# Performance work log

Measured on AMD Instinct MI355X. Metric: run time of the kernel, lower is better.

## Reference

```python
import jax, jax.numpy as jnp
import numpy as np

IN_F = 128
OUT_F = 128
ALPHA = 0.2  # LeakyReLU negative slope


def _xavier_uniform(key, shape, gain):
    fan_in, fan_out = shape[0], shape[1]
    bound = gain * np.sqrt(6.0 / (fan_in + fan_out))
    return jax.random.uniform(key, shape, jnp.float32, -bound, bound)


def setup_inputs() -> dict:
    key = jax.random.key(0)
    kx, kw, ka = jax.random.split(key, 3)
    x = jax.random.normal(kx, (8, 2048, IN_F), jnp.float32)
    W = _xavier_uniform(kw, (IN_F, OUT_F), 1.414)
    a = _xavier_uniform(ka, (2 * OUT_F, 1), 1.414)
    return {"x": x, "W": W, "a": a}


def reference(x, W, a):
    B, T, _ = x.shape
    h = jnp.matmul(x, W)  # [B, T, F]
    # e_ij = leakyrelu([h_i ; h_j] @ a) = leakyrelu(h_i @ a1 + h_j @ a2)
    a1 = a[:OUT_F, 0]   # [F]
    a2 = a[OUT_F:, 0]   # [F]
    f1 = h @ a1         # [B, T]
    f2 = h @ a2         # [B, T]
    e = f1[:, :, None] + f2[:, None, :]          # [B, T, T]
    e = jnp.where(e >= 0, e, ALPHA * e)          # LeakyReLU
    attention = jax.nn.softmax(e, axis=-1)       # [B, T, T]
    # dropout is identity at inference
    return jnp.matmul(attention, h)              # [B, T, F]
```

## Files before the change

kernel.cpp:

```cpp
#include <hip/hip_runtime.h>
#include <hip/hip_bf16.h>

typedef __attribute__((ext_vector_type(8))) short short8;
typedef __attribute__((ext_vector_type(8))) unsigned short ushort8;
typedef __attribute__((ext_vector_type(16))) float f32x16;

#define LOG2E 1.4426950408889634f
#define MFMA32(a, b, c) __builtin_amdgcn_mfma_f32_32x32x16_bf16((a), (b), (c), 0, 0, 0)
#define ZERO16 {0.f,0.f,0.f,0.f,0.f,0.f,0.f,0.f,0.f,0.f,0.f,0.f,0.f,0.f,0.f,0.f}

__device__ __forceinline__ unsigned short bfbits(float f) {
    __hip_bfloat16 h = __float2bfloat16(f);
    return __builtin_bit_cast(unsigned short, h);
}
__device__ __forceinline__ float bf2f(unsigned short u) {
    unsigned v = ((unsigned)u) << 16;
    return __builtin_bit_cast(float, v);
}

__global__ __launch_bounds__(256) void gat_wt(const float* __restrict__ W,
                                              unsigned short* __restrict__ WT2h,
                                              unsigned short* __restrict__ WT2l,
                                              unsigned int* __restrict__ f2mk) {
    if (blockIdx.x == 0 && threadIdx.x < 8) f2mk[threadIdx.x] = 0u;
    const int k16 = blockIdx.x;
    const int d = threadIdx.x >> 1;
    const int klo8 = (threadIdx.x & 1) * 8;
    ushort8 vh, vl;
#pragma unroll
    for (int q = 0; q < 8; ++q) {
        float f = W[(k16 * 16 + klo8 + q) * 128 + d];
        unsigned short hb = bfbits(f);
        vh[q] = hb;
        vl[q] = bfbits(f - bf2f(hb));
    }
    size_t base = (size_t)k16 * 2048 + d * 16 + klo8;
    *(ushort8*)(WT2h + base) = vh;
    *(ushort8*)(WT2l + base) = vl;
}

__global__ __launch_bounds__(256) void gat_h(const float* __restrict__ x,
                                             const unsigned short* __restrict__ WT2h,
                                             const unsigned short* __restrict__ WT2l,
                                             const float* __restrict__ a,
                                             unsigned short* __restrict__ HT2h,
                                             float* __restrict__ f1l,
                                             float* __restrict__ f2l,
                                             unsigned int* __restrict__ f2mk) {
    __shared__ unsigned short xs_h[32][132];
    __shared__ unsigned short xs_l[32][132];
    __shared__ float hs[32][130];
    __shared__ float red[2][32][8];
    const int tid = threadIdx.x;
    const int lane = tid & 63;
    const int wv = tid >> 6;
    const int l31 = lane & 31;
    const int hi = lane >> 5;
    const int t0 = blockIdx.x * 32;
    const int c0 = wv * 32;

#pragma unroll
    for (int r8 = 0; r8 < 4; ++r8) {
        int row = r8 * 8 + (tid >> 5);
        int c4 = (tid & 31) * 4;
        float4 v = *(const float4*)(x + (size_t)(t0 + row) * 128 + c4);
        float f[4] = {v.x, v.y, v.z, v.w};
#pragma unroll
        for (int q = 0; q < 4; ++q) {
            unsigned short hb = bfbits(f[q]);
            xs_h[row][c4 + q] = hb;
            xs_l[row][c4 + q] = bfbits(f[q] - bf2f(hb));
        }
    }
    __syncthreads();

    f32x16 p0 = ZERO16, p1 = ZERO16, p2 = ZERO16;
    const unsigned short* bph = WT2h + (c0 + l31) * 16 + 8 * hi;
    const unsigned short* bpl = WT2l + (c0 + l31) * 16 + 8 * hi;
#pragma unroll
    for (int kk8 = 0; kk8 < 8; ++kk8) {
        short8 ah = *(const short8*)&xs_h[l31][kk8 * 16 + 8 * hi];
        short8 al = *(const short8*)&xs_l[l31][kk8 * 16 + 8 * hi];
        short8 bh = __builtin_bit_cast(short8, *(const ushort8*)(bph + kk8 * 2048));
        short8 bl = __builtin_bit_cast(short8, *(const ushort8*)(bpl + kk8 * 2048));
        p0 = MFMA32(ah, bh, p0);
        p1 = MFMA32(al, bh, p1);
        p2 = MFMA32(ah, bl, p2);
    }
#pragma unroll
    for (int r = 0; r < 16; ++r) {
        int crow = (r & 3) + 8 * (r >> 2) + 4 * hi;
        hs[crow][c0 + l31] = p0[r] + p1[r] + p2[r];
    }
    __syncthreads();
    {
        const int d = tid & 127, half = tid >> 7;
        ushort8 h0, h1;
#pragma unroll
        for (int j = 0; j < 8; ++j) h0[j] = bfbits(hs[half * 16 + j][d]);
#pragma unroll
        for (int j = 0; j < 8; ++j) h1[j] = bfbits(hs[half * 16 + 8 + j][d]);
        const int b = t0 >> 11;
        const int tloc = t0 & 2047;
        size_t base = (size_t)b * 262144 + (size_t)(tloc / 16 + half) * 2048 + d * 16;
        *(ushort8*)(HT2h + base) = h0;
        *(ushort8*)(HT2h + base + 8) = h1;
    }
    {
        const int r = tid & 31, seg = tid >> 5;
        float s1 = 0.f, s2 = 0.f;
#pragma unroll
        for (int i = 0; i < 16; ++i) {
            float hv = hs[r][seg * 16 + i];
            s1 += hv * a[seg * 16 + i];
            s2 += hv * a[128 + seg * 16 + i];
        }
        red[0][r][seg] = s1;
        red[1][r][seg] = s2;
    }
    __syncthreads();
    if (tid < 32) {
        float s1 = 0.f, s2 = 0.f;
#pragma unroll
        for (int g = 0; g < 8; ++g) { s1 += red[0][tid][g]; s2 += red[1][tid][g]; }
        f1l[t0 + tid] = s1 * LOG2E;
        float f2v = s2 * LOG2E;
        f2l[t0 + tid] = f2v;
        float m = f2v;
#pragma unroll
        for (int o = 1; o < 32; o <<= 1) m = fmaxf(m, __shfl_xor(m, o, 32));
        if (tid == 0) {
            unsigned int bits = __builtin_bit_cast(unsigned int, m);
            unsigned int key = (bits & 0x80000000u) ? ~bits : (bits | 0x80000000u);
            atomicMax(f2mk + (t0 >> 11), key);
        }
    }
}

__global__ __launch_bounds__(512, 2) void gat_attn(const unsigned short* __restrict__ HT2h,
                                                   const float* __restrict__ f1l,
                                                   const float* __restrict__ f2l,
                                                   const unsigned int* __restrict__ f2mk,
                                                   float* __restrict__ out) {
    __shared__ float lred[4][64][132];
    __shared__ float sps[8][64];
    __shared__ float sinv[64];
    const int bid = blockIdx.x;
    const int b = bid & 7;
    const int tile = bid >> 3;
    const int tid = threadIdx.x;
    const int lane = tid & 63;
    const int wv = tid >> 6;
    const int l31 = lane & 31;
    const int hi = lane >> 5;
    const int koff = hi * 8;

    const unsigned int kk = f2mk[b];
    const unsigned int mbits = (kk & 0x80000000u) ? (kk & 0x7fffffffu) : ~kk;
    const float fm = __builtin_bit_cast(float, mbits);

    const int rowg = b * 2048 + tile * 64 + l31;
    const float f1m0 = f1l[rowg];
    const float f1m1 = f1l[rowg + 32];
    const float tm0 = f1m0 + fm, tm1 = f1m1 + fm;
    const float ml0 = fmaxf(tm0, 0.2f * tm0);
    const float ml1 = fmaxf(tm1, 0.2f * tm1);
    const float A0 = f1m0 - ml0, B0 = 0.2f * f1m0 - ml0;
    const float A1 = f1m1 - ml1, B1 = 0.2f * f1m1 - ml1;

    const int jbase = wv * 256;
    const float* f2b = f2l + b * 2048 + jbase;
    const unsigned short* ph = HT2h + (size_t)b * 262144
                             + (size_t)(jbase >> 4) * 2048 + l31 * 16 + koff;

    f32x16 acc[2][4] = {{ZERO16, ZERO16, ZERO16, ZERO16},
                        {ZERO16, ZERO16, ZERO16, ZERO16}};
    float sp0 = 0.f, sp1 = 0.f;

    uint4 vh0 = *(const uint4*)(ph);
    uint4 vh1 = *(const uint4*)(ph + 512);
    uint4 vh2 = *(const uint4*)(ph + 1024);
    uint4 vh3 = *(const uint4*)(ph + 1536);

    for (int it = 0; it < 16; ++it) {
        const unsigned short* pn = ph + (size_t)((it + 1) & 15) * 2048;
        uint4 nh0 = *(const uint4*)(pn);
        uint4 nh1 = *(const uint4*)(pn + 512);
        uint4 nh2 = *(const uint4*)(pn + 1024);
        uint4 nh3 = *(const uint4*)(pn + 1536);
        float4 fva = *(const float4*)(f2b + it * 16 + koff);
        float4 fvb = *(const float4*)(f2b + it * 16 + koff + 4);

        float fv[8] = {fva.x, fva.y, fva.z, fva.w, fvb.x, fvb.y, fvb.z, fvb.w};
        short8 af0, af1;
#pragma unroll
        for (int q = 0; q < 8; ++q) {
            float g = 0.2f * fv[q];
            float p0 = __builtin_amdgcn_exp2f(fmaxf(A0 + fv[q], B0 + g));
            float p1 = __builtin_amdgcn_exp2f(fmaxf(A1 + fv[q], B1 + g));
            sp0 += p0; sp1 += p1;
            af0[q] = (short)bfbits(p0);
            af1[q] = (short)bfbits(p1);
        }
        acc[0][0] = MFMA32(af0, __builtin_bit_cast(short8, vh0), acc[0][0]);
        acc[0][1] = MFMA32(af0, __builtin_bit_cast(short8, vh1), acc[0][1]);
        acc[0][2] = MFMA32(af0, __builtin_bit_cast(short8, vh2), acc[0][2]);
        acc[0][3] = MFMA32(af0, __builtin_bit_cast(short8, vh3), acc[0][3]);
        acc[1][0] = MFMA32(af1, __builtin_bit_cast(short8, vh0), acc[1][0]);
        acc[1][1] = MFMA32(af1, __builtin_bit_cast(short8, vh1), acc[1][1]);
        acc[1][2] = MFMA32(af1, __builtin_bit_cast(short8, vh2), acc[1][2]);
        acc[1][3] = MFMA32(af1, __builtin_bit_cast(short8, vh3), acc[1][3]);

        vh0 = nh0; vh1 = nh1; vh2 = nh2; vh3 = nh3;
    }

    sp0 += __shfl_xor(sp0, 32, 64);
    sp1 += __shfl_xor(sp1, 32, 64);
    if (lane < 32) { sps[wv][l31] = sp0; sps[wv][32 + l31] = sp1; }

    if (wv >= 4) {
#pragma unroll
        for (int r = 0; r < 16; ++r) {
            int crow = (r & 3) + 8 * (r >> 2) + 4 * hi;
#pragma unroll
            for (int s = 0; s < 2; ++s)
#pragma unroll
                for (int c = 0; c < 4; ++c)
                    lred[wv - 4][s * 32 + crow][c * 32 + l31] = acc[s][c][r];
        }
    }
    __syncthreads();
    if (wv < 4) {
#pragma unroll
        for (int r = 0; r < 16; ++r) {
            int crow = (r & 3) + 8 * (r >> 2) + 4 * hi;
#pragma unroll
            for (int s = 0; s < 2; ++s)
#pragma unroll
                for (int c = 0; c < 4; ++c)
                    acc[s][c][r] += lred[wv][s * 32 + crow][c * 32 + l31];
        }
    } else if (wv == 4) {
        float tot = 0.f;
#pragma unroll
        for (int w = 0; w < 8; ++w) tot += sps[w][lane];
        sinv[lane] = 1.0f / tot;
    }
    __syncthreads();
    if (wv == 2 || wv == 3) {
#pragma unroll
        for (int r = 0; r < 16; ++r) {
            int crow = (r & 3) + 8 * (r >> 2) + 4 * hi;
#pragma unroll
            for (int s = 0; s < 2; ++s)
#pragma unroll
                for (int c = 0; c < 4; ++c)
                    lred[wv - 2][s * 32 + crow][c * 32 + l31] = acc[s][c][r];
        }
    }
    __syncthreads();
    if (wv < 2) {
#pragma unroll
        for (int r = 0; r < 16; ++r) {
            int crow = (r & 3) + 8 * (r >> 2) + 4 * hi;
#pragma unroll
            for (int s = 0; s < 2; ++s)
#pragma unroll
                for (int c = 0; c < 4; ++c)
                    acc[s][c][r] += lred[wv][s * 32 + crow][c * 32 + l31];
        }
    }
    __syncthreads();
    if (wv == 1) {
#pragma unroll
        for (int r = 0; r < 16; ++r) {
            int crow = (r & 3) + 8 * (r >> 2) + 4 * hi;
#pragma unroll
            for (int s = 0; s < 2; ++s)
#pragma unroll
                for (int c = 0; c < 4; ++c)
                    lred[0][s * 32 + crow][c * 32 + l31] = acc[s][c][r];
        }
    }
    __syncthreads();
    if (wv == 0) {
        const size_t obase = ((size_t)b * 2048 + (size_t)tile * 64) * 128;
#pragma unroll
        for (int r = 0; r < 16; ++r) {
            int crow = (r & 3) + 8 * (r >> 2) + 4 * hi;
#pragma unroll
            for (int s = 0; s < 2; ++s) {
                int row = s * 32 + crow;
                float iv = sinv[row];
#pragma unroll
                for (int c = 0; c < 4; ++c) {
                    float v = acc[s][c][r] + lred[0][row][c * 32 + l31];
                    out[obase + (size_t)row * 128 + c * 32 + l31] = v * iv;
                }
            }
        }
    }
}

extern "C" void kernel_launch(void* const* d_in, const int* in_sizes, int n_in,
                              void* d_out, int out_size, void* d_ws, size_t ws_size,
                              hipStream_t stream) {
    const float* x = (const float*)d_in[0];
    const float* W = (const float*)d_in[1];
    const float* a = (const float*)d_in[2];
    float* out = (float*)d_out;

    unsigned short* WT2h = (unsigned short*)d_ws;
    unsigned short* WT2l = WT2h + 128 * 128;
    unsigned short* HT2h = WT2l + 128 * 128;
    float* f1l = (float*)(HT2h + (size_t)8 * 128 * 2048);
    float* f2l = f1l + 16384;
    unsigned int* f2mk = (unsigned int*)(f2l + 16384);

    gat_wt<<<8, 256, 0, stream>>>(W, WT2h, WT2l, f2mk);
    gat_h<<<512, 256, 0, stream>>>(x, WT2h, WT2l, a, HT2h, f1l, f2l, f2mk);
    gat_attn<<<256, 512, 0, stream>>>(HT2h, f1l, f2l, f2mk, out);
}
```

Measured before the change: 40.16 us.

## Stage f2 in LDS and double-buffer H loads across two unrolled iterations

The f2 row vector is copied once per block into shared memory so the inner loop reads it from LDS instead of global memory. The main loop is unrolled by two with separate X/Y register buffers, prefetching H two steps ahead and interleaving exp generation with MFMA issue. The lred padding is also dropped from 132 to 128, which may bring LDS bank conflicts back in the reduction. The aim is to hide global load latency and overlap VALU exp work with matrix ops, at the cost of more registers and extra LDS.

```diff
diff --git a/kernel.cpp b/kernel.cpp
--- a/kernel.cpp
+++ b/kernel.cpp
@@ -137,12 +137,29 @@
     }
 }
 
+__device__ __forceinline__ void gen_af(float4 fa, float4 fb,
+                                       float A0, float B0, float A1, float B1,
+                                       float& sp0, float& sp1,
+                                       short8& af0, short8& af1) {
+    float fv[8] = {fa.x, fa.y, fa.z, fa.w, fb.x, fb.y, fb.z, fb.w};
+#pragma unroll
+    for (int q = 0; q < 8; ++q) {
+        float g = 0.2f * fv[q];
+        float p0 = __builtin_amdgcn_exp2f(fmaxf(A0 + fv[q], B0 + g));
+        float p1 = __builtin_amdgcn_exp2f(fmaxf(A1 + fv[q], B1 + g));
+        sp0 += p0; sp1 += p1;
+        af0[q] = (short)bfbits(p0);
+        af1[q] = (short)bfbits(p1);
+    }
+}
+
 __global__ __launch_bounds__(512, 2) void gat_attn(const unsigned short* __restrict__ HT2h,
                                                    const float* __restrict__ f1l,
                                                    const float* __restrict__ f2l,
                                                    const unsigned int* __restrict__ f2mk,
                                                    float* __restrict__ out) {
-    __shared__ float lred[4][64][132];
+    __shared__ float lred[4][64][128];
+    __shared__ float f2s[2048];
     __shared__ float sps[8][64];
     __shared__ float sinv[64];
     const int bid = blockIdx.x;
@@ -155,6 +172,8 @@
     const int hi = lane >> 5;
     const int koff = hi * 8;
 
+    *(float4*)(f2s + tid * 4) = *(const float4*)(f2l + b * 2048 + tid * 4);
+
     const unsigned int kk = f2mk[b];
     const unsigned int mbits = (kk & 0x80000000u) ? (kk & 0x7fffffffu) : ~kk;
     const float fm = __builtin_bit_cast(float, mbits);
@@ -168,50 +187,71 @@
     const float A0 = f1m0 - ml0, B0 = 0.2f * f1m0 - ml0;
     const float A1 = f1m1 - ml1, B1 = 0.2f * f1m1 - ml1;
 
-    const int jbase = wv * 256;
-    const float* f2b = f2l + b * 2048 + jbase;
-    const unsigned short* ph = HT2h + (size_t)b * 262144
-                             + (size_t)(jbase >> 4) * 2048 + l31 * 16 + koff;
+    const int jloc = wv * 256;
+    const unsigned short* phg = HT2h + (size_t)b * 262144
+                              + (size_t)(jloc >> 4) * 2048 + l31 * 16 + koff;
 
     f32x16 acc[2][4] = {{ZERO16, ZERO16, ZERO16, ZERO16},
                         {ZERO16, ZERO16, ZERO16, ZERO16}};
     float sp0 = 0.f, sp1 = 0.f;
 
-    uint4 vh0 = *(const uint4*)(ph);
-    uint4 vh1 = *(const uint4*)(ph + 512);
-    uint4 vh2 = *(const uint4*)(ph + 1024);
-    uint4 vh3 = *(const uint4*)(ph + 1536);
-
-    for (int it = 0; it < 16; ++it) {
-        const unsigned short* pn = ph + (size_t)((it + 1) & 15) * 2048;
-        uint4 nh0 = *(const uint4*)(pn);
-        uint4 nh1 = *(const uint4*)(pn + 512);
-        uint4 nh2 = *(const uint4*)(pn + 1024);
-        uint4 nh3 = *(const uint4*)(pn + 1536);
-        float4 fva = *(const float4*)(f2b + it * 16 + koff);
-        float4 fvb = *(const float4*)(f2b + it * 16 + koff + 4);
-
-        float fv[8] = {fva.x, fva.y, fva.z, fva.w, fvb.x, fvb.y, fvb.z, fvb.w};
+    uint4 X0 = *(const uint4*)(phg);
+    uint4 X1 = *(const uint4*)(phg + 512);
+    uint4 X2 = *(const uint4*)(phg + 1024);
+    uint4 X3 = *(const uint4*)(phg + 1536);
+    uint4 Y0 = *(const uint4*)(phg + 2048);
+    uint4 Y1 = *(const uint4*)(phg + 2048 + 512);
+    uint4 Y2 = *(const uint4*)(phg + 2048 + 1024);
+    uint4 Y3 = *(const uint4*)(phg + 2048 + 1536);
+
+    __syncthreads();
+
+    float4 fA0 = *(const float4*)(f2s + jloc + koff);
+    float4 fA1 = *(const float4*)(f2s + jloc + koff + 4);
+
+    for (int it2 = 0; it2 < 8; ++it2) {
+        const int itE = it2 * 2, itO = it2 * 2 + 1;
         short8 af0, af1;
-#pragma unroll
-        for (int q = 0; q < 8; ++q) {
-            float g = 0.2f * fv[q];
-            float p0 = __builtin_amdgcn_exp2f(fmaxf(A0 + fv[q], B0 + g));
-            float p1 = __builtin_amdgcn_exp2f(fmaxf(A1 + fv[q], B1 + g));
-            sp0 += p0; sp1 += p1;
-            af0[q] = (short)bfbits(p0);
-            af1[q] = (short)bfbits(p1);
-        }
-        acc[0][0] = MFMA32(af0, __builtin_bit_cast(short8, vh0), acc[0][0]);
-        acc[0][1] = MFMA32(af0, __builtin_bit_cast(short8, vh1), acc[0][1]);
-        acc[0][2] = MFMA32(af0, __builtin_bit_cast(short8, vh2), acc[0][2]);
-        acc[0][3] = MFMA32(af0, __builtin_bit_cast(short8, vh3), acc[0][3]);
-        acc[1][0] = MFMA32(af1, __builtin_bit_cast(short8, vh0), acc[1][0]);
-        acc[1][1] = MFMA32(af1, __builtin_bit_cast(short8, vh1), acc[1][1]);
-        acc[1][2] = MFMA32(af1, __builtin_bit_cast(short8, vh2), acc[1][2]);
-        acc[1][3] = MFMA32(af1, __builtin_bit_cast(short8, vh3), acc[1][3]);
-
-        vh0 = nh0; vh1 = nh1; vh2 = nh2; vh3 = nh3;
+        gen_af(fA0, fA1, A0, B0, A1, B1, sp0, sp1, af0, af1);
+        float4 fB0 = *(const float4*)(f2s + jloc + itO * 16 + koff);
+        float4 fB1 = *(const float4*)(f2s + jloc + itO * 16 + koff + 4);
+        acc[0][0] = MFMA32(af0, __builtin_bit_cast(short8, X0), acc[0][0]);
+        acc[0][1] = MFMA32(af0, __builtin_bit_cast(short8, X1), acc[0][1]);
+        acc[0][2] = MFMA32(af0, __builtin_bit_cast(short8, X2), acc[0][2]);
+        acc[0][3] = MFMA32(af0, __builtin_bit_cast(short8, X3), acc[0][3]);
+        acc[1][0] = MFMA32(af1, __builtin_bit_cast(short8, X0), acc[1][0]);
+        acc[1][1] = MFMA32(af1, __builtin_bit_cast(short8, X1), acc[1][1]);
+        acc[1][2] = MFMA32(af1, __builtin_bit_cast(short8, X2), acc[1][2]);
+        acc[1][3] = MFMA32(af1, __builtin_bit_cast(short8, X3), acc[1][3]);
+        {
+            const unsigned short* pn = phg + (size_t)((itE + 2) & 15) * 2048;
+            X0 = *(const uint4*)(pn);
+            X1 = *(const uint4*)(pn + 512);
+            X2 = *(const uint4*)(pn + 1024);
+            X3 = *(const uint4*)(pn + 1536);
+        }
+        short8 bf0, bf1;
+        gen_af(fB0, fB1, A0, B0, A1, B1, sp0, sp1, bf0, bf1);
+        {
+            const int itN = (itO + 1) & 15;
+            fA0 = *(const float4*)(f2s + jloc + itN * 16 + koff);
+            fA1 = *(const float4*)(f2s + jloc + itN * 16 + koff + 4);
+        }
+        acc[0][0] = MFMA32(bf0, __builtin_bit_cast(short8, Y0), acc[0][0]);
+        acc[0][1] = MFMA32(bf0, __builtin_bit_cast(short8, Y1), acc[0][1]);
+        acc[0][2] = MFMA32(bf0, __builtin_bit_cast(short8, Y2), acc[0][2]);
+        acc[0][3] = MFMA32(bf0, __builtin_bit_cast(short8, Y3), acc[0][3]);
+        acc[1][0] = MFMA32(bf1, __builtin_bit_cast(short8, Y0), acc[1][0]);
+        acc[1][1] = MFMA32(bf1, __builtin_bit_cast(short8, Y1), acc[1][1]);
+        acc[1][2] = MFMA32(bf1, __builtin_bit_cast(short8, Y2), acc[1][2]);
+        acc[1][3] = MFMA32(bf1, __builtin_bit_cast(short8, Y3), acc[1][3]);
+        {
+            const unsigned short* pn = phg + (size_t)((itO + 2) & 15) * 2048;
+            Y0 = *(const uint4*)(pn);
+            Y1 = *(const uint4*)(pn + 512);
+            Y2 = *(const uint4*)(pn + 1024);
+            Y3 = *(const uint4*)(pn + 1536);
+        }
     }
 
     sp0 += __shfl_xor(sp0, 32, 64);
```

After: 38.89 us. -3.2%, faster.

## Stream H tiles through LDS with async global_load_lds ring buffer

Applied to the files above, without the earlier changes.

Replaces the per-wave register double-buffered global loads of the H tiles with a 4-deep ring of direct global-to-LDS async loads (global_load_lds), gated by vmcnt waits. It also stages the f2 logits for the batch into shared memory once per block, and reuses the new 128KB shared buffer for the cross-wave reduction. The aim is to hide global-memory latency deeper and cut register pressure. The costs are much larger LDS use (about 140KB per block), which may block the two-blocks-per-CU target, plus an extra barrier. There is also a risk that the slot being refilled is overwritten while its LDS reads may still be in flight.

```diff
diff --git a/kernel.cpp b/kernel.cpp
--- a/kernel.cpp
+++ b/kernel.cpp
@@ -16,6 +16,12 @@
 __device__ __forceinline__ float bf2f(unsigned short u) {
     unsigned v = ((unsigned)u) << 16;
     return __builtin_bit_cast(float, v);
+}
+
+typedef unsigned int __attribute__((address_space(1))) as1_u32;
+typedef unsigned int __attribute__((address_space(3))) as3_u32;
+__device__ __forceinline__ void gload_lds16(const void* g, void* l) {
+    __builtin_amdgcn_global_load_lds((const as1_u32*)g, (as3_u32*)l, 16, 0, 0);
 }
 
 __global__ __launch_bounds__(256) void gat_wt(const float* __restrict__ W,
@@ -137,12 +143,29 @@
     }
 }
 
+__device__ __forceinline__ void gen_af(float4 fa, float4 fb,
+                                       float A0, float B0, float A1, float B1,
+                                       float& sp0, float& sp1,
+                                       short8& af0, short8& af1) {
+    float fv[8] = {fa.x, fa.y, fa.z, fa.w, fb.x, fb.y, fb.z, fb.w};
+#pragma unroll
+    for (int q = 0; q < 8; ++q) {
+        float g = 0.2f * fv[q];
+        float p0 = __builtin_amdgcn_exp2f(fmaxf(A0 + fv[q], B0 + g));
+        float p1 = __builtin_amdgcn_exp2f(fmaxf(A1 + fv[q], B1 + g));
+        sp0 += p0; sp1 += p1;
+        af0[q] = (short)bfbits(p0);
+        af1[q] = (short)bfbits(p1);
+    }
+}
+
 __global__ __launch_bounds__(512, 2) void gat_attn(const unsigned short* __restrict__ HT2h,
                                                    const float* __restrict__ f1l,
                                                    const float* __restrict__ f2l,
                                                    const unsigned int* __restrict__ f2mk,
                                                    float* __restrict__ out) {
-    __shared__ float lred[4][64][132];
+    __shared__ __align__(16) unsigned char smem[131072];
+    __shared__ float f2s[2048];
     __shared__ float sps[8][64];
     __shared__ float sinv[64];
     const int bid = blockIdx.x;
@@ -155,6 +178,8 @@
     const int hi = lane >> 5;
     const int koff = hi * 8;
 
+    *(float4*)(f2s + tid * 4) = *(const float4*)(f2l + b * 2048 + tid * 4);
+
     const unsigned int kk = f2mk[b];
     const unsigned int mbits = (kk & 0x80000000u) ? (kk & 0x7fffffffu) : ~kk;
     const float fm = __builtin_bit_cast(float, mbits);
@@ -168,55 +193,59 @@
     const float A0 = f1m0 - ml0, B0 = 0.2f * f1m0 - ml0;
     const float A1 = f1m1 - ml1, B1 = 0.2f * f1m1 - ml1;
 
-    const int jbase = wv * 256;
-    const float* f2b = f2l + b * 2048 + jbase;
-    const unsigned short* ph = HT2h + (size_t)b * 262144
-                             + (size_t)(jbase >> 4) * 2048 + l31 * 16 + koff;
+    const int jloc = wv * 256;
+    const unsigned short* gbase = HT2h + (size_t)b * 262144 + (size_t)(jloc >> 4) * 2048
+                                + l31 * 16 + koff;
+    unsigned short* sbase = (unsigned short*)smem + wv * 8192;
+
+    __syncthreads();
+
+#pragma unroll
+    for (int g = 0; g < 4; ++g) {
+#pragma unroll
+        for (int c = 0; c < 4; ++c)
+            gload_lds16(gbase + (size_t)g * 2048 + c * 512, sbase + g * 2048 + c * 512);
+    }
 
     f32x16 acc[2][4] = {{ZERO16, ZERO16, ZERO16, ZERO16},
                         {ZERO16, ZERO16, ZERO16, ZERO16}};
     float sp0 = 0.f, sp1 = 0.f;
 
-    uint4 vh0 = *(const uint4*)(ph);
-    uint4 vh1 = *(const uint4*)(ph + 512);
-    uint4 vh2 = *(const uint4*)(ph + 1024);
-    uint4 vh3 = *(const uint4*)(ph + 1536);
-
-    for (int it = 0; it < 16; ++it) {
-        const unsigned short* pn = ph + (size_t)((it + 1) & 15) * 2048;
-        uint4 nh0 = *(const uint4*)(pn);
-        uint4 nh1 = *(const uint4*)(pn + 512);
-        uint4 nh2 = *(const uint4*)(pn + 1024);
-        uint4 nh3 = *(const uint4*)(pn + 1536);
-        float4 fva = *(const float4*)(f2b + it * 16 + koff);
-        float4 fvb = *(const float4*)(f2b + it * 16 + koff + 4);
-
-        float fv[8] = {fva.x, fva.y, fva.z, fva.w, fvb.x, fvb.y, fvb.z, fvb.w};
+    for (int i = 0; i < 16; ++i) {
+        asm volatile("s_waitcnt vmcnt(12)" ::: "memory");
+        __builtin_amdgcn_sched_barrier(0);
+        const unsigned short* rp = sbase + (i & 3) * 2048 + lane * 8;
+        uint4 v0 = *(const uint4*)(rp);
+        uint4 v1 = *(const uint4*)(rp + 512);
+        uint4 v2 = *(const uint4*)(rp + 1024);
+        uint4 v3 = *(const uint4*)(rp + 1536);
+        float4 fa = *(const float4*)(f2s + jloc + i * 16 + koff);
+        float4 fb = *(const float4*)(f2s + jloc + i * 16 + koff + 4);
         short8 af0, af1;
-#pragma unroll
-        for (int q = 0; q < 8; ++q) {
-            float g = 0.2f * fv[q];
-            float p0 = __builtin_amdgcn_exp2f(fmaxf(A0 + fv[q], B0 + g));
-            float p1 = __builtin_amdgcn_exp2f(fmaxf(A1 + fv[q], B1 + g));
-            sp0 += p0; sp1 += p1;
-            af0[q] = (short)bfbits(p0);
-            af1[q] = (short)bfbits(p1);
-        }
-        acc[0][0] = MFMA32(af0, __builtin_bit_cast(short8, vh0), acc[0][0]);
-        acc[0][1] = MFMA32(af0, __builtin_bit_cast(short8, vh1), acc[0][1]);
-        acc[0][2] = MFMA32(af0, __builtin_bit_cast(short8, vh2), acc[0][2]);
-        acc[0][3] = MFMA32(af0, __builtin_bit_cast(short8, vh3), acc[0][3]);
-        acc[1][0] = MFMA32(af1, __builtin_bit_cast(short8, vh0), acc[1][0]);
-        acc[1][1] = MFMA32(af1, __builtin_bit_cast(short8, vh1), acc[1][1]);
-        acc[1][2] = MFMA32(af1, __builtin_bit_cast(short8, vh2), acc[1][2]);
-        acc[1][3] = MFMA32(af1, __builtin_bit_cast(short8, vh3), acc[1][3]);
-
-        vh0 = nh0; vh1 = nh1; vh2 = nh2; vh3 = nh3;
+        gen_af(fa, fb, A0, B0, A1, B1, sp0, sp1, af0, af1);
+        acc[0][0] = MFMA32(af0, __builtin_bit_cast(short8, v0), acc[0][0]);
+        acc[0][1] = MFMA32(af0, __builtin_bit_cast(short8, v1), acc[0][1]);
+        acc[0][2] = MFMA32(af0, __builtin_bit_cast(short8, v2), acc[0][2]);
+        acc[0][3] = MFMA32(af0, __builtin_bit_cast(short8, v3), acc[0][3]);
+        acc[1][0] = MFMA32(af1, __builtin_bit_cast(short8, v0), acc[1][0]);
+        acc[1][1] = MFMA32(af1, __builtin_bit_cast(short8, v1), acc[1][1]);
+        acc[1][2] = MFMA32(af1, __builtin_bit_cast(short8, v2), acc[1][2]);
+        acc[1][3] = MFMA32(af1, __builtin_bit_cast(short8, v3), acc[1][3]);
+        __builtin_amdgcn_sched_barrier(0);
+        const unsigned short* gsrc = gbase + (size_t)((i + 4) & 15) * 2048;
+        unsigned short* ld = sbase + (i & 3) * 2048;
+#pragma unroll
+        for (int c = 0; c < 4; ++c)
+            gload_lds16(gsrc + c * 512, ld + c * 512);
     }
 
     sp0 += __shfl_xor(sp0, 32, 64);
     sp1 += __shfl_xor(sp1, 32, 64);
     if (lane < 32) { sps[wv][l31] = sp0; sps[wv][32 + l31] = sp1; }
+
+    __syncthreads();
+
+    float (*lred)[64][128] = (float (*)[64][128])smem;
 
     if (wv >= 4) {
 #pragma unroll
```

Measured after the change: 41.56 us. +3.5%, slower.

## Fuse W split into gat_h and halve attention row tile to double grid

Applied to the files above, without the earlier changes.

Removes the separate W transpose/split kernel: each gat_h thread now loads its slice of W directly and splits it into bf16 hi/lo in registers, replacing that launch with a memset. The attention kernel now processes 32 query rows per block instead of 64, doubling the grid to 512 blocks, raising the occupancy hint to 4 blocks per CU, and staging f2 in LDS. This trades more parallelism and lower register and LDS use for re-reading the H stream twice as often, and every gat_h block redundantly re-reading W from global memory.

```diff
diff --git a/kernel.cpp b/kernel.cpp
--- a/kernel.cpp
+++ b/kernel.cpp
@@ -18,30 +18,8 @@
     return __builtin_bit_cast(float, v);
 }
 
-__global__ __launch_bounds__(256) void gat_wt(const float* __restrict__ W,
-                                              unsigned short* __restrict__ WT2h,
-                                              unsigned short* __restrict__ WT2l,
-                                              unsigned int* __restrict__ f2mk) {
-    if (blockIdx.x == 0 && threadIdx.x < 8) f2mk[threadIdx.x] = 0u;
-    const int k16 = blockIdx.x;
-    const int d = threadIdx.x >> 1;
-    const int klo8 = (threadIdx.x & 1) * 8;
-    ushort8 vh, vl;
-#pragma unroll
-    for (int q = 0; q < 8; ++q) {
-        float f = W[(k16 * 16 + klo8 + q) * 128 + d];
-        unsigned short hb = bfbits(f);
-        vh[q] = hb;
-        vl[q] = bfbits(f - bf2f(hb));
-    }
-    size_t base = (size_t)k16 * 2048 + d * 16 + klo8;
-    *(ushort8*)(WT2h + base) = vh;
-    *(ushort8*)(WT2l + base) = vl;
-}
-
 __global__ __launch_bounds__(256) void gat_h(const float* __restrict__ x,
-                                             const unsigned short* __restrict__ WT2h,
-                                             const unsigned short* __restrict__ WT2l,
+                                             const float* __restrict__ W,
                                              const float* __restrict__ a,
                                              unsigned short* __restrict__ HT2h,
                                              float* __restrict__ f1l,
@@ -59,6 +37,13 @@
     const int t0 = blockIdx.x * 32;
     const int c0 = wv * 32;
 
+    float wf[64];
+#pragma unroll
+    for (int kk8 = 0; kk8 < 8; ++kk8)
+#pragma unroll
+        for (int q = 0; q < 8; ++q)
+            wf[kk8 * 8 + q] = W[(kk8 * 16 + 8 * hi + q) * 128 + c0 + l31];
+
 #pragma unroll
     for (int r8 = 0; r8 < 4; ++r8) {
         int row = r8 * 8 + (tid >> 5);
@@ -72,20 +57,27 @@
             xs_l[row][c4 + q] = bfbits(f[q] - bf2f(hb));
         }
     }
+
+    short8 wh[8], wl[8];
+#pragma unroll
+    for (int kk8 = 0; kk8 < 8; ++kk8)
+#pragma unroll
+        for (int q = 0; q < 8; ++q) {
+            float f = wf[kk8 * 8 + q];
+            unsigned short hb = bfbits(f);
+            wh[kk8][q] = (short)hb;
+            wl[kk8][q] = (short)bfbits(f - bf2f(hb));
+        }
     __syncthreads();
 
     f32x16 p0 = ZERO16, p1 = ZERO16, p2 = ZERO16;
-    const unsigned short* bph = WT2h + (c0 + l31) * 16 + 8 * hi;
-    const unsigned short* bpl = WT2l + (c0 + l31) * 16 + 8 * hi;
 #pragma unroll
     for (int kk8 = 0; kk8 < 8; ++kk8) {
         short8 ah = *(const short8*)&xs_h[l31][kk8 * 16 + 8 * hi];
         short8 al = *(const short8*)&xs_l[l31][kk8 * 16 + 8 * hi];
-        short8 bh = __builtin_bit_cast(short8, *(const ushort8*)(bph + kk8 * 2048));
-        short8 bl = __builtin_bit_cast(short8, *(const ushort8*)(bpl + kk8 * 2048));
-        p0 = MFMA32(ah, bh, p0);
-        p1 = MFMA32(al, bh, p1);
-        p2 = MFMA32(ah, bl, p2);
+        p0 = MFMA32(ah, wh[kk8], p0);
+        p1 = MFMA32(al, wh[kk8], p1);
+        p2 = MFMA32(ah, wl[kk8], p2);
     }
 #pragma unroll
     for (int r = 0; r < 16; ++r) {
@@ -137,14 +129,15 @@
     }
 }
 
-__global__ __launch_bounds__(512, 2) void gat_attn(const unsigned short* __restrict__ HT2h,
+__global__ __launch_bounds__(512, 4) void gat_attn(const unsigned short* __restrict__ HT2h,
                                                    const float* __restrict__ f1l,
                                                    const float* __restrict__ f2l,
                                                    const unsigned int* __restrict__ f2mk,
                                                    float* __restrict__ out) {
-    __shared__ float lred[4][64][132];
-    __shared__ float sps[8][64];
-    __shared__ float sinv[64];
+    __shared__ float lred[4][32][128];
+    __shared__ float f2s[2048];
+    __shared__ float sps[8][32];
+    __shared__ float sinv[32];
     const int bid = blockIdx.x;
     const int b = bid & 7;
     const int tile = bid >> 3;
@@ -155,78 +148,67 @@
     const int hi = lane >> 5;
     const int koff = hi * 8;
 
+    *(float4*)(f2s + tid * 4) = *(const float4*)(f2l + b * 2048 + tid * 4);
+
     const unsigned int kk = f2mk[b];
     const unsigned int mbits = (kk & 0x80000000u) ? (kk & 0x7fffffffu) : ~kk;
     const float fm = __builtin_bit_cast(float, mbits);
 
-    const int rowg = b * 2048 + tile * 64 + l31;
-    const float f1m0 = f1l[rowg];
-    const float f1m1 = f1l[rowg + 32];
-    const float tm0 = f1m0 + fm, tm1 = f1m1 + fm;
-    const float ml0 = fmaxf(tm0, 0.2f * tm0);
-    const float ml1 = fmaxf(tm1, 0.2f * tm1);
-    const float A0 = f1m0 - ml0, B0 = 0.2f * f1m0 - ml0;
-    const float A1 = f1m1 - ml1, B1 = 0.2f * f1m1 - ml1;
-
-    const int jbase = wv * 256;
-    const float* f2b = f2l + b * 2048 + jbase;
-    const unsigned short* ph = HT2h + (size_t)b * 262144
-                             + (size_t)(jbase >> 4) * 2048 + l31 * 16 + koff;
-
-    f32x16 acc[2][4] = {{ZERO16, ZERO16, ZERO16, ZERO16},
-                        {ZERO16, ZERO16, ZERO16, ZERO16}};
-    float sp0 = 0.f, sp1 = 0.f;
-
-    uint4 vh0 = *(const uint4*)(ph);
-    uint4 vh1 = *(const uint4*)(ph + 512);
-    uint4 vh2 = *(const uint4*)(ph + 1024);
-    uint4 vh3 = *(const uint4*)(ph + 1536);
-
-    for (int it = 0; it < 16; ++it) {
-        const unsigned short* pn = ph + (size_t)((it + 1) & 15) * 2048;
-        uint4 nh0 = *(const uint4*)(pn);
-        uint4 nh1 = *(const uint4*)(pn + 512);
-        uint4 nh2 = *(const uint4*)(pn + 1024);
-        uint4 nh3 = *(const uint4*)(pn + 1536);
-        float4 fva = *(const float4*)(f2b + it * 16 + koff);
-        float4 fvb = *(const float4*)(f2b + it * 16 + koff + 4);
-
-        float fv[8] = {fva.x, fva.y, fva.z, fva.w, fvb.x, fvb.y, fvb.z, fvb.w};
-        short8 af0, af1;
+    const float f1m = f1l[b * 2048 + tile * 32 + l31];
+    const float tm = f1m + fm;
+    const float ml = fmaxf(tm, 0.2f * tm);
+    const float A0 = f1m - ml, B0 = 0.2f * f1m - ml;
+
+    const int jloc = wv * 256;
+    const unsigned short* gbase = HT2h + (size_t)b * 262144
+                                + (size_t)(jloc >> 4) * 2048 + l31 * 16 + koff;
+
+    f32x16 acc0 = ZERO16, acc1 = ZERO16, acc2 = ZERO16, acc3 = ZERO16;
+    float sp = 0.f;
+
+    uint4 X0 = *(const uint4*)(gbase);
+    uint4 X1 = *(const uint4*)(gbase + 512);
+    uint4 X2 = *(const uint4*)(gbase + 1024);
+    uint4 X3 = *(const uint4*)(gbase + 1536);
+
+    __syncthreads();
+
+    for (int i = 0; i < 16; ++i) {
+        float4 fa = *(const float4*)(f2s + jloc + i * 16 + koff);
+        float4 fb = *(const float4*)(f2s + jloc + i * 16 + koff + 4);
+        const unsigned short* pn = gbase + (size_t)((i + 1) & 15) * 2048;
+        uint4 N0 = *(const uint4*)(pn);
+        uint4 N1 = *(const uint4*)(pn + 512);
+        uint4 N2 = *(const uint4*)(pn + 1024);
+        uint4 N3 = *(const uint4*)(pn + 1536);
+
+        float fv[8] = {fa.x, fa.y, fa.z, fa.w, fb.x, fb.y, fb.z, fb.w};
+        short8 af;
 #pragma unroll
         for (int q = 0; q < 8; ++q) {
             float g = 0.2f * fv[q];
-            float p0 = __builtin_amdgcn_exp2f(fmaxf(A0 + fv[q], B0 + g));
-            float p1 = __builtin_amdgcn_exp2f(fmaxf(A1 + fv[q], B1 + g));
-            sp0 += p0; sp1 += p1;
-            af0[q] = (short)bfbits(p0);
-            af1[q] = (short)bfbits(p1);
-        }
-        acc[0][0] = MFMA32(af0, __builtin_bit_cast(short8, vh0), acc[0][0]);
-        acc[0][1] = MFMA32(af0, __builtin_bit_cast(short8, vh1), acc[0][1]);
-        acc[0][2] = MFMA32(af0, __builtin_bit_cast(short8, vh2), acc[0][2]);
-        acc[0][3] = MFMA32(af0, __builtin_bit_cast(short8, vh3), acc[0][3]);
-        acc[1][0] = MFMA32(af1, __builtin_bit_cast(short8, vh0), acc[1][0]);
-        acc[1][1] = MFMA32(af1, __builtin_bit_cast(short8, vh1), acc[1][1]);
-        acc[1][2] = MFMA32(af1, __builtin_bit_cast(short8, vh2), acc[1][2]);
-        acc[1][3] = MFMA32(af1, __builtin_bit_cast(short8, vh3), acc[1][3]);
-
-        vh0 = nh0; vh1 = nh1; vh2 = nh2; vh3 = nh3;
-    }
-
-    sp0 += __shfl_xor(sp0, 32, 64);
-    sp1 += __shfl_xor(sp1, 32, 64);
-    if (lane < 32) { sps[wv][l31] = sp0; sps[wv][32 + l31] = sp1; }
+            float p = __builtin_amdgcn_exp2f(fmaxf(A0 + fv[q], B0 + g));
+            sp += p;
+            af[q] = (short)bfbits(p);
+        }
+        acc0 = MFMA32(af, __builtin_bit_cast(short8, X0), acc0);
+        acc1 = MFMA32(af, __builtin_bit_cast(short8, X1), acc1);
+        acc2 = MFMA32(af, __builtin_bit_cast(short8, X2), acc2);
+        acc3 = MFMA32(af, __builtin_bit_cast(short8, X3), acc3);
+        X0 = N0; X1 = N1; X2 = N2; X3 = N3;
+    }
+
+    sp += __shfl_xor(sp, 32, 64);
+    if (lane < 32) sps[wv][l31] = sp;
 
     if (wv >= 4) {
 #pragma unroll
         for (int r = 0; r < 16; ++r) {
             int crow = (r & 3) + 8 * (r >> 2) + 4 * hi;
-#pragma unroll
-            for (int s = 0; s < 2; ++s)
-#pragma unroll
-                for (int c = 0; c < 4; ++c)
-                    lred[wv - 4][s * 32 + crow][c * 32 + l31] = acc[s][c][r];
+            lred[wv - 4][crow][l31] = acc0[r];
+            lred[wv - 4][crow][32 + l31] = acc1[r];
+            lred[wv - 4][crow][64 + l31] = acc2[r];
+            lred[wv - 4][crow][96 + l31] = acc3[r];
         }
     }
     __syncthreads();
@@ -234,28 +216,28 @@
 #pragma unroll
         for (int r = 0; r < 16; ++r) {
             int crow = (r & 3) + 8 * (r >> 2) + 4 * hi;
-#pragma unroll
-            for (int s = 0; s < 2; ++s)
-#pragma unroll
-                for (int c = 0; c < 4; ++c)
-                    acc[s][c][r] += lred[wv][s * 32 + crow][c * 32 + l31];
+            acc0[r] += lred[wv][crow][l31];
+            acc1[r] += lred[wv][crow][32 + l31];
+            acc2[r] += lred[wv][crow][64 + l31];
+            acc3[r] += lred[wv][crow][96 + l31];
         }
     } else if (wv == 4) {
-        float tot = 0.f;
-#pragma unroll
-        for (int w = 0; w < 8; ++w) tot += sps[w][lane];
-        sinv[lane] = 1.0f / tot;
+        if (lane < 32) {
+            float tot = 0.f;
+#pragma unroll
+            for (int w = 0; w < 8; ++w) tot += sps[w][l31];
+            sinv[l31] = 1.0f / tot;
+        }
     }
     __syncthreads();
     if (wv == 2 || wv == 3) {
 #pragma unroll
         for (int r = 0; r < 16; ++r) {
             int crow = (r & 3) + 8 * (r >> 2) + 4 * hi;
-#pragma unroll
-            for (int s = 0; s < 2; ++s)
-#pragma unroll
-                for (int c = 0; c < 4; ++c)
-                    lred[wv - 2][s * 32 + crow][c * 32 + l31] = acc[s][c][r];
+            lred[wv - 2][crow][l31] = acc0[r];
+            lred[wv - 2][crow][32 + l31] = acc1[r];
+            lred[wv - 2][crow][64 + l31] = acc2[r];
+            lred[wv - 2][crow][96 + l31] = acc3[r];
         }
     }
     __syncthreads();
@@ -263,11 +245,10 @@
 #pragma unroll
         for (int r = 0; r < 16; ++r) {
             int crow = (r & 3) + 8 * (r >> 2) + 4 * hi;
-#pragma unroll
-            for (int s = 0; s < 2; ++s)
-#pragma unroll
-                for (int c = 0; c < 4; ++c)
-                    acc[s][c][r] += lred[wv][s * 32 + crow][c * 32 + l31];
+            acc0[r] += lred[wv][crow][l31];
+            acc1[r] += lred[wv][crow][32 + l31];
+            acc2[r] += lred[wv][crow][64 + l31];
+            acc3[r] += lred[wv][crow][96 + l31];
         }
     }
     __syncthreads();
@@ -275,29 +256,23 @@
 #pragma unroll
         for (int r = 0; r < 16; ++r) {
             int crow = (r & 3) + 8 * (r >> 2) + 4 * hi;
-#pragma unroll
-            for (int s = 0; s < 2; ++s)
-#pragma unroll
-                for (int c = 0; c < 4; ++c)
-                    lred[0][s * 32 + crow][c * 32 + l31] = acc[s][c][r];
+            lred[0][crow][l31] = acc0[r];
+            lred[0][crow][32 + l31] = acc1[r];
+            lred[0][crow][64 + l31] = acc2[r];
+            lred[0][crow][96 + l31] = acc3[r];
         }
     }
     __syncthreads();
     if (wv == 0) {
-        const size_t obase = ((size_t)b * 2048 + (size_t)tile * 64) * 128;
-#pragma unroll
-        for (int r = 0; r < 16; ++r) {
-            int crow = (r & 3) + 8 * (r >> 2) + 4 * hi;
-#pragma unroll
-            for (int s = 0; s < 2; ++s) {
-                int row = s * 32 + crow;
-                float iv = sinv[row];
-#pragma unroll
-                for (int c = 0; c < 4; ++c) {
-                    float v = acc[s][c][r] + lred[0][row][c * 32 + l31];
-                    out[obase + (size_t)row * 128 + c * 32 + l31] = v * iv;
-                }
-            }
+        const size_t obase = ((size_t)b * 2048 + (size_t)tile * 32) * 128;
+#pragma unroll
+        for (int r = 0; r < 16; ++r) {
+            int crow = (r & 3) + 8 * (r >> 2) + 4 * hi;
+            float iv = sinv[crow];
+            out[obase + (size_t)crow * 128 + l31]       = (acc0[r] + lred[0][crow][l31]) * iv;
+            out[obase + (size_t)crow * 128 + 32 + l31]  = (acc1[r] + lred[0][crow][32 + l31]) * iv;
+            out[obase + (size_t)crow * 128 + 64 + l31]  = (acc2[r] + lred[0][crow][64 + l31]) * iv;
+            out[obase + (size_t)crow * 128 + 96 + l31]  = (acc3[r] + lred[0][crow][96 + l31]) * iv;
         }
     }
 }
@@ -310,14 +285,12 @@
     const float* a = (const float*)d_in[2];
     float* out = (float*)d_out;
 
-    unsigned short* WT2h = (unsigned short*)d_ws;
-    unsigned short* WT2l = WT2h + 128 * 128;
-    unsigned short* HT2h = WT2l + 128 * 128;
+    unsigned short* HT2h = (unsigned short*)d_ws;
     float* f1l = (float*)(HT2h + (size_t)8 * 128 * 2048);
     float* f2l = f1l + 16384;
     unsigned int* f2mk = (unsigned int*)(f2l + 16384);
 
-    gat_wt<<<8, 256, 0, stream>>>(W, WT2h, WT2l, f2mk);
-    gat_h<<<512, 256, 0, stream>>>(x, WT2h, WT2l, a, HT2h, f1l, f2l, f2mk);
-    gat_attn<<<256, 512, 0, stream>>>(HT2h, f1l, f2l, f2mk, out);
-}
+    hipMemsetAsync(f2mk, 0, 8 * sizeof(unsigned int), stream);
+    gat_h<<<512, 256, 0, stream>>>(x, W, a, HT2h, f1l, f2l, f2mk);
+    gat_attn<<<512, 512, 0, stream>>>(HT2h, f1l, f2l, f2mk, out);
+}
```

Result: faster. 39.24 us (-2.3%).
